# Optimization experiments

Hardware: AMD Instinct MI355X
Metric: run time of the kernel (lower is better)

Reference implementation:

```python
import jax, jax.numpy as jnp
import numpy as np


def setup_inputs() -> dict:
    key = jax.random.key(0)
    B, C, H, W = 16, 512, 56, 56
    heads, agent, win = 8, 49, 56
    ks = jax.random.split(key, 16)
    std = 0.02
    tn = lambda k, s: jax.random.truncated_normal(k, -2.0, 2.0, s, jnp.float32) * std
    return {
        "x": jax.random.normal(ks[0], (B, C, H, W), jnp.float32),
        "H": H,
        "W": W,
        "q_w": jax.random.normal(ks[1], (C, C), jnp.float32) * (C ** -0.5),
        "kv_w": jax.random.normal(ks[2], (2 * C, C), jnp.float32) * (C ** -0.5),
        "proj_w": jax.random.normal(ks[3], (C, C), jnp.float32) * (C ** -0.5),
        "proj_b": jnp.zeros((C,), jnp.float32),
        "dwc_w": jax.random.normal(ks[4], (C, 1, 3, 3), jnp.float32) * (1.0 / 3.0),
        "dwc_b": jnp.zeros((C,), jnp.float32),
        "an_bias": tn(ks[5], (heads, agent, 7, 7)),
        "na_bias": tn(ks[6], (heads, agent, 7, 7)),
        "ah_bias": tn(ks[7], (1, heads, agent, win, 1)),
        "aw_bias": tn(ks[8], (1, heads, agent, 1, win)),
        "ha_bias": tn(ks[9], (1, heads, win, 1, agent)),
        "wa_bias": tn(ks[10], (1, heads, 1, win, agent)),
    }


def reference(x, H, W, q_w, kv_w, proj_w, proj_b, dwc_w, dwc_b,
              an_bias, na_bias, ah_bias, aw_bias, ha_bias, wa_bias):
    B, C, H1, W1 = x.shape
    heads, agent = an_bias.shape[0], an_bias.shape[1]
    hd = C // heads
    scale = hd ** -0.5
    n = H1 * W1
    pool = int(agent ** 0.5)  # 7

    # NOTE: original torch code does x.view(B, H1*W1, C) on an NCHW tensor:
    # a raw row-major reshape, reproduced faithfully here.
    xf = x.reshape(B, n, C)

    q = xf @ q_w.T                       # [B, n, C]
    kv = xf @ kv_w.T                     # [B, n, 2C]
    k, v = kv[..., :C], kv[..., C:]

    # agent tokens: adaptive avg pool of q (as HxW image) to pool x pool (exact blocks)
    q_img = q.reshape(B, H, W, C)
    agent_tokens = q_img.reshape(B, pool, H // pool, pool, W // pool, C).mean(axis=(2, 4))
    agent_tokens = agent_tokens.reshape(B, agent, C)

    qh = q.reshape(B, n, heads, hd).transpose(0, 2, 1, 3)            # [B,h,n,d]
    kh = k.reshape(B, n, heads, hd).transpose(0, 2, 1, 3)            # [B,h,n,d]
    vh = v.reshape(B, n, heads, hd).transpose(0, 2, 1, 3)            # [B,h,n,d]
    ah = agent_tokens.reshape(B, agent, heads, hd).transpose(0, 2, 1, 3)  # [B,h,a,d]

    # stage 1: agent -> kv attention, with interpolated + separable position bias
    pb1 = jax.image.resize(an_bias, (heads, agent, H, W), 'bilinear').reshape(1, heads, agent, n)
    pb2 = (ah_bias + aw_bias).reshape(1, heads, agent, n)
    agent_logits = jnp.einsum('bhad,bhnd->bhan', ah * scale, kh) + pb1 + pb2
    agent_attn = jax.nn.softmax(agent_logits, axis=-1)
    agent_v = jnp.einsum('bhan,bhnd->bhad', agent_attn, vh)          # [B,h,a,d]

    # stage 2: query -> agent attention
    ab1 = jax.image.resize(na_bias, (heads, agent, H, W), 'bilinear').reshape(1, heads, agent, n)
    ab1 = ab1.transpose(0, 1, 3, 2)                                  # [1,h,n,a]
    ab2 = (ha_bias + wa_bias).reshape(1, heads, n, agent)
    q_logits = jnp.einsum('bhnd,bhad->bhna', qh * scale, ah) + ab1 + ab2
    q_attn = jax.nn.softmax(q_logits, axis=-1)
    out = jnp.einsum('bhna,bhad->bhnd', q_attn, agent_v)
    out = out.transpose(0, 2, 1, 3).reshape(B, n, C)

    # depthwise-conv residual on v (sr_ratio == 1: no interpolate)
    v_img = v.reshape(B, H, W, C).transpose(0, 3, 1, 2)              # [B,C,H,W]
    dwc = jax.lax.conv_general_dilated(
        v_img, dwc_w, window_strides=(1, 1), padding='SAME',
        feature_group_count=C, dimension_numbers=('NCHW', 'OIHW', 'NCHW'))
    dwc = dwc + dwc_b[None, :, None, None]
    out = out + dwc.transpose(0, 2, 3, 1).reshape(B, n, C)

    out = out @ proj_w.T + proj_b
    return out.reshape(B, C, H1, W1)
```

## Files before the change

kernel.cpp:

```cpp
#include <hip/hip_runtime.h>
#include <math.h>

#define B_ 16
#define C_ 512
#define Nn 3136
#define HEADS 8
#define HD 64
#define AG 49
#define Mrows (B_ * Nn)

typedef unsigned short ushortT;
typedef __attribute__((ext_vector_type(8))) short bf16x8;
typedef __attribute__((ext_vector_type(4))) float f32x4;

#define MFMA16(a, b, c) __builtin_amdgcn_mfma_f32_16x16x32_bf16((a), (b), (c), 0, 0, 0)

__device__ inline float bf2f(ushortT u) { return __uint_as_float(((unsigned)u) << 16); }
__device__ inline ushortT f2bf(float f) {
    unsigned x = __float_as_uint(f);
    unsigned r = (x + 0x7fffu + ((x >> 16) & 1u)) >> 16;
    return (ushortT)r;
}
__device__ inline f32x4 fzero4() { f32x4 z = {0.f, 0.f, 0.f, 0.f}; return z; }

__device__ inline void gl_lds16(const ushortT* g, ushortT* l) {
    __builtin_amdgcn_global_load_lds(
        (const __attribute__((address_space(1))) void*)g,
        (__attribute__((address_space(3))) void*)l, 16, 0, 0);
}

#define VMCNT(n) asm volatile("s_waitcnt vmcnt(" #n ")" ::: "memory")
#define LGKM0_SB() { asm volatile("s_waitcnt lgkmcnt(0)" ::: "memory"); \
                     __builtin_amdgcn_sched_barrier(0); }
#define BAR() __builtin_amdgcn_s_barrier()

__global__ void cvt_weights(const float* __restrict__ qw, const float* __restrict__ kvw,
                            const float* __restrict__ pw, const float* __restrict__ dwcw,
                            ushortT* __restrict__ Wqkv, ushortT* __restrict__ Wp,
                            float* __restrict__ wT) {
    int g = blockIdx.x * 256 + threadIdx.x;
    if (g < 196608) {
        const float* src = (g < 65536) ? &qw[(size_t)g * 4] : &kvw[(size_t)(g - 65536) * 4];
        float4 v = *(const float4*)src;
        *(ushort4*)&Wqkv[(size_t)g * 4] =
            make_ushort4(f2bf(v.x), f2bf(v.y), f2bf(v.z), f2bf(v.w));
    } else if (g < 262144) {
        float4 v = *(const float4*)&pw[(size_t)(g - 196608) * 4];
        *(ushort4*)&Wp[(size_t)(g - 196608) * 4] =
            make_ushort4(f2bf(v.x), f2bf(v.y), f2bf(v.z), f2bf(v.w));
    } else {
        int gg = g - 262144;
        if (gg < 4608) { int c = gg & 511, tap = gg >> 9; wT[gg] = dwcw[c * 9 + tap]; }
    }
}

template <int MB, int NL>
__device__ __forceinline__ void quad(f32x4 (&acc)[8][4], const bf16x8 (&af)[4][2],
                                     const bf16x8 (&bf)[4][2]) {
#pragma unroll
    for (int m = 0; m < 4; ++m)
#pragma unroll
        for (int n = 0; n < 2; ++n) {
            acc[MB + m][NL + n] = MFMA16(af[m][0], bf[NL + n][0], acc[MB + m][NL + n]);
            acc[MB + m][NL + n] = MFMA16(af[m][1], bf[NL + n][1], acc[MB + m][NL + n]);
        }
}

__global__ __launch_bounds__(512, 2)
void gemm_f32a(const float* __restrict__ A32, const ushortT* __restrict__ Bw,
               ushortT* __restrict__ out, int N, int nbn) {
    __shared__ __align__(16) ushortT As[2][16384];
    __shared__ __align__(16) ushortT Bs[2][16384];
    const int t = threadIdx.x, lane = t & 63, wid = t >> 6;
    const int chunk = (int)gridDim.x >> 3;
    const int id2 = ((int)blockIdx.x & 7) * chunk + ((int)blockIdx.x >> 3);
    const int by = id2 / nbn, bx = id2 - by * nbn;
    const int m0 = by * 256, n0 = bx * 256;
    const int wm = wid >> 2, wn = wid & 3;

    const int rl0 = t >> 3;
    const int kg = t & 7;
    const int wkg = kg ^ (rl0 & 7);
    const float* gAr = A32 + (size_t)(m0 + rl0) * 512 + kg * 8;
    const int dA0 = rl0 * 64 + wkg * 8;
    const int rb0 = (rl0 & 31) + ((rl0 >> 5) << 6);
    const int rb1 = rb0 + 128;
    const ushortT* gB0 = Bw + (size_t)(n0 + rb0) * 512 + wkg * 8;
    const ushortT* gB1 = Bw + (size_t)(n0 + rb1) * 512 + wkg * 8;
    const int gbu = ((wid * 8) & 31) + (((wid * 8) >> 5) << 6);
    const int bB0 = gbu * 64;
    const int bB1 = bB0 + 8192;

#define ISSB(bufi, ro, ko) { gl_lds16(gB0 + (ro) * 512 + (ko), &Bs[bufi][bB0 + (ro) * 64]); \
                             gl_lds16(gB1 + (ro) * 512 + (ko), &Bs[bufi][bB1 + (ro) * 64]); }
#define CVTW(bufi) { \
    _Pragma("unroll") \
    for (int j = 0; j < 4; ++j) { \
        bf16x8 w; \
        w[0]=(short)f2bf(pa[j][0].x); w[1]=(short)f2bf(pa[j][0].y); \
        w[2]=(short)f2bf(pa[j][0].z); w[3]=(short)f2bf(pa[j][0].w); \
        w[4]=(short)f2bf(pa[j][1].x); w[5]=(short)f2bf(pa[j][1].y); \
        w[6]=(short)f2bf(pa[j][1].z); w[7]=(short)f2bf(pa[j][1].w); \
        *(bf16x8*)&As[bufi][dA0 + j * 4096] = w; \
    } }

    f32x4 acc[8][4];
#pragma unroll
    for (int i = 0; i < 8; ++i)
#pragma unroll
        for (int j = 0; j < 4; ++j) acc[i][j] = fzero4();

    const int r15 = lane & 15, kq16 = lane >> 4;
    const int rA = wm * 128 + r15;
    const int rB = wn * 64 + r15;
    const int sw0 = ((kq16) ^ (r15 & 7)) << 3;
    const int sw1 = ((4 + kq16) ^ (r15 & 7)) << 3;

    float4 pa[4][2];
#pragma unroll
    for (int j = 0; j < 4; ++j) {
        const float* s = gAr + (size_t)j * 64 * 512;
        pa[j][0] = *(const float4*)s; pa[j][1] = *(const float4*)(s + 4);
    }
    ISSB(0, 0, 0); ISSB(0, 32, 0);
    CVTW(0);
    __syncthreads();

    bf16x8 af[4][2], bf[4][2];
    int cur = 0;
    for (int kt = 0; kt < 8; ++kt) {
        const ushortT* Ac = As[cur];
        const ushortT* Bc = Bs[cur];
        const int nb = cur ^ 1;
        const int ko = (kt + 1) * 64;
        const bool pre = (kt < 7);
        if (pre) {
#pragma unroll
            for (int j = 0; j < 4; ++j) {
                const float* s = gAr + (size_t)j * 64 * 512 + ko;
                pa[j][0] = *(const float4*)s; pa[j][1] = *(const float4*)(s + 4);
            }
            ISSB(nb, 0, ko); ISSB(nb, 32, ko);
        }
#pragma unroll
        for (int mt = 0; mt < 4; ++mt) {
            af[mt][0] = *(const bf16x8*)&Ac[(rA + mt * 16) * 64 + sw0];
            af[mt][1] = *(const bf16x8*)&Ac[(rA + mt * 16) * 64 + sw1];
        }
#pragma unroll
        for (int nt = 0; nt < 2; ++nt) {
            bf[nt][0] = *(const bf16x8*)&Bc[(rB + nt * 16) * 64 + sw0];
            bf[nt][1] = *(const bf16x8*)&Bc[(rB + nt * 16) * 64 + sw1];
        }
        __builtin_amdgcn_s_setprio(1);
        quad<0, 0>(acc, af, bf);
        __builtin_amdgcn_s_setprio(0);
#pragma unroll
        for (int nt = 2; nt < 4; ++nt) {
            bf[nt][0] = *(const bf16x8*)&Bc[(rB + nt * 16) * 64 + sw0];
            bf[nt][1] = *(const bf16x8*)&Bc[(rB + nt * 16) * 64 + sw1];
        }
        __builtin_amdgcn_s_setprio(1);
        quad<0, 2>(acc, af, bf);
        __builtin_amdgcn_s_setprio(0);
#pragma unroll
        for (int mt = 0; mt < 4; ++mt) {
            af[mt][0] = *(const bf16x8*)&Ac[(rA + 64 + mt * 16) * 64 + sw0];
            af[mt][1] = *(const bf16x8*)&Ac[(rA + 64 + mt * 16) * 64 + sw1];
        }
        __builtin_amdgcn_s_setprio(1);
        quad<4, 0>(acc, af, bf);
        quad<4, 2>(acc, af, bf);
        __builtin_amdgcn_s_setprio(0);
        if (pre) { CVTW(nb); }
        __syncthreads();
        cur ^= 1;
    }
#undef ISSB
#undef CVTW

    const int cn = r15, rg = kq16 << 2;
#pragma unroll
    for (int mt = 0; mt < 8; ++mt) {
        int mrow = m0 + wm * 128 + mt * 16 + rg;
#pragma unroll
        for (int nt = 0; nt < 4; ++nt) {
            int ncol = n0 + wn * 64 + nt * 16 + cn;
#pragma unroll
            for (int r = 0; r < 4; ++r)
                out[(size_t)(mrow + r) * N + ncol] = f2bf(acc[mt][nt][r]);
        }
    }
}

template <typename TO>
__global__ __launch_bounds__(512, 2)
void gemm256(const ushortT* __restrict__ A, const ushortT* __restrict__ Bw,
             const float* __restrict__ bias, TO* __restrict__ out,
             int N, int nbn) {
    __shared__ __align__(16) ushortT As[2][16384];
    __shared__ __align__(16) ushortT Bs[2][16384];
    const int t = threadIdx.x, lane = t & 63, wid = t >> 6;
    const int chunk = (int)gridDim.x >> 3;
    const int id2 = ((int)blockIdx.x & 7) * chunk + ((int)blockIdx.x >> 3);
    const int by = id2 / nbn, bx = id2 - by * nbn;
    const int m0 = by * 256, n0 = bx * 256;
    const int wm = wid >> 2, wn = wid & 3;

    const int rl0 = t >> 3;
    const int skg = (t & 7) ^ (rl0 & 7);
    const int ra0 = rl0 & 63;
    const int ra1 = (rl0 & 63) + 128;
    const int rb0 = (rl0 & 31) + ((rl0 >> 5) << 6);
    const int rb1 = rb0 + 128;
    const ushortT* gA0 = A + (size_t)(m0 + ra0) * 512 + skg * 8;
    const ushortT* gA1 = A + (size_t)(m0 + ra1) * 512 + skg * 8;
    const ushortT* gB0 = Bw + (size_t)(n0 + rb0) * 512 + skg * 8;
    const ushortT* gB1 = Bw + (size_t)(n0 + rb1) * 512 + skg * 8;
    const int bA0 = wid * 512;
    const int bA1 = wid * 512 + 8192;
    const int gbu = ((wid * 8) & 31) + (((wid * 8) >> 5) << 6);
    const int bB0 = gbu * 64;
    const int bB1 = bB0 + 8192;

#define ISSA(bufi, ro, ko) { gl_lds16(gA0 + (ro) * 512 + (ko), &As[bufi][bA0 + (ro) * 64]); \
                             gl_lds16(gA1 + (ro) * 512 + (ko), &As[bufi][bA1 + (ro) * 64]); }
#define ISSB(bufi, ro, ko) { gl_lds16(gB0 + (ro) * 512 + (ko), &Bs[bufi][bB0 + (ro) * 64]); \
                             gl_lds16(gB1 + (ro) * 512 + (ko), &Bs[bufi][bB1 + (ro) * 64]); }

    f32x4 acc[8][4];
#pragma unroll
    for (int i = 0; i < 8; ++i)
#pragma unroll
        for (int j = 0; j < 4; ++j) acc[i][j] = fzero4();

    const int r15 = lane & 15, kq16 = lane >> 4;
    const int rA = wm * 128 + r15;
    const int rB = wn * 64 + r15;
    const int sw0 = ((kq16) ^ (r15 & 7)) << 3;
    const int sw1 = ((4 + kq16) ^ (r15 & 7)) << 3;

    ISSA(0, 0, 0); ISSA(0, 64, 0);
    ISSB(0, 0, 0); ISSB(0, 32, 0);
    VMCNT(0);
    BAR();

    bf16x8 af[4][2], bf[4][2];
    for (int kt = 0; kt < 8; ++kt) {
        const ushortT* Ac = As[kt & 1];
        const ushortT* Bc = Bs[kt & 1];
        const int nb = (kt + 1) & 1;
        const int ko = (kt + 1) * 64;
        const bool pre = (kt < 7);
#pragma unroll
        for (int mt = 0; mt < 4; ++mt) {
            af[mt][0] = *(const bf16x8*)&Ac[(rA + mt * 16) * 64 + sw0];
            af[mt][1] = *(const bf16x8*)&Ac[(rA + mt * 16) * 64 + sw1];
        }
#pragma unroll
        for (int nt = 0; nt < 2; ++nt) {
            bf[nt][0] = *(const bf16x8*)&Bc[(rB + nt * 16) * 64 + sw0];
            bf[nt][1] = *(const bf16x8*)&Bc[(rB + nt * 16) * 64 + sw1];
        }
        if (pre) { ISSA(nb, 0, ko); ISSA(nb, 64, ko); }
        BAR(); LGKM0_SB();
        __builtin_amdgcn_s_setprio(1);
        quad<0, 0>(acc, af, bf);
        __builtin_amdgcn_s_setprio(0);
        BAR();
#pragma unroll
        for (int nt = 2; nt < 4; ++nt) {
            bf[nt][0] = *(const bf16x8*)&Bc[(rB + nt * 16) * 64 + sw0];
            bf[nt][1] = *(const bf16x8*)&Bc[(rB + nt * 16) * 64 + sw1];
        }
        if (pre) { ISSB(nb, 0, ko); ISSB(nb, 32, ko); }
        BAR(); LGKM0_SB();
        __builtin_amdgcn_s_setprio(1);
        quad<0, 2>(acc, af, bf);
        __builtin_amdgcn_s_setprio(0);
        BAR();
#pragma unroll
        for (int mt = 0; mt < 4; ++mt) {
            af[mt][0] = *(const bf16x8*)&Ac[(rA + 64 + mt * 16) * 64 + sw0];
            af[mt][1] = *(const bf16x8*)&Ac[(rA + 64 + mt * 16) * 64 + sw1];
        }
        BAR(); LGKM0_SB();
        __builtin_amdgcn_s_setprio(1);
        quad<4, 0>(acc, af, bf);
        __builtin_amdgcn_s_setprio(0);
        BAR();
        __builtin_amdgcn_s_setprio(1);
        quad<4, 2>(acc, af, bf);
        __builtin_amdgcn_s_setprio(0);
        if (pre) { VMCNT(0); }
        BAR();
    }
#undef ISSA
#undef ISSB

    const int cn = r15, rg = kq16 << 2;
#pragma unroll
    for (int mt = 0; mt < 8; ++mt) {
        int mrow = m0 + wm * 128 + mt * 16 + rg;
#pragma unroll
        for (int nt = 0; nt < 4; ++nt) {
            int ncol = n0 + wn * 64 + nt * 16 + cn;
            float bv = bias ? bias[ncol] : 0.f;
#pragma unroll
            for (int r = 0; r < 4; ++r) {
                float v = acc[mt][nt][r] + bv;
                if (sizeof(TO) == 2) ((ushortT*)out)[(size_t)(mrow + r) * N + ncol] = f2bf(v);
                else                 ((float*)out)[(size_t)(mrow + r) * N + ncol] = v;
            }
        }
    }
}

__global__ __launch_bounds__(256)
void agent_pool(const ushortT* __restrict__ qkv, float* __restrict__ at) {
    __shared__ float red[256][9];
    int t = threadIdx.x;
    int ba = blockIdx.x;
    int b = ba / AG, a = ba % AG;
    int c8 = (t & 63) << 3, qr = t >> 6;
    int p1 = a / 7, p2 = a % 7;
    float s[8] = {};
#pragma unroll
    for (int pp = 0; pp < 16; ++pp) {
        int pos = (qr << 4) + pp;
        int i = (p1 * 8 + (pos >> 3)) * 56 + p2 * 8 + (pos & 7);
        bf16x8 u = *(const bf16x8*)&qkv[(size_t)(b * Nn + i) * 1536 + c8];
#pragma unroll
        for (int j = 0; j < 8; ++j) s[j] += bf2f((ushortT)u[j]);
    }
#pragma unroll
    for (int j = 0; j < 8; ++j) red[t][j] = s[j];
    __syncthreads();
    if (t < 64) {
        float* o = &at[((size_t)(b * AG + a) << 9) + (t << 3)];
#pragma unroll
        for (int j = 0; j < 8; ++j)
            o[j] = (red[t][j] + red[t + 64][j] + red[t + 128][j] + red[t + 192][j])
                   * (1.f / 64.f);
    }
}

__device__ inline float bilin7(const float* __restrict__ p, int y, int x) {
    float fy = fminf(fmaxf(y * 0.125f - 0.4375f, 0.f), 6.f);
    float fx = fminf(fmaxf(x * 0.125f - 0.4375f, 0.f), 6.f);
    int y0 = (int)fy; float ty = fy - y0; int y1 = min(y0 + 1, 6);
    int x0 = (int)fx; float tx = fx - x0; int x1 = min(x0 + 1, 6);
    float v00 = p[y0 * 7 + x0], v01 = p[y0 * 7 + x1];
    float v10 = p[y1 * 7 + x0], v11 = p[y1 * 7 + x1];
    return (1.f - ty) * ((1.f - tx) * v00 + tx * v01) + ty * ((1.f - tx) * v10 + tx * v11);
}

__global__ void bias_k(const float* __restrict__ an, const float* __restrict__ ahb,
                       const float* __restrict__ awb, const float* __restrict__ na,
                       const float* __restrict__ hab, const float* __restrict__ wab,
                       ushortT* __restrict__ b1, ushortT* __restrict__ b2) {
    int g = blockIdx.x * 256 + threadIdx.x;
    const int NT = HEADS * AG * Nn;
    if (g < NT) {
        int i = g % Nn; int a = (g / Nn) % AG; int h = g / (AG * Nn);
        int y = i / 56, x = i % 56;
        b1[g] = f2bf(bilin7(an + (h * AG + a) * 49, y, x)
                     + ahb[(h * AG + a) * 56 + y] + awb[(h * AG + a) * 56 + x]);
    } else {
        g -= NT; if (g >= NT) return;
        int a = g % AG; int i = (g / AG) % Nn; int h = g / (AG * Nn);
        int y = i / 56, x = i % 56;
        b2[g] = f2bf(bilin7(na + (h * AG + a) * 49, y, x)
                     + hab[(h * 56 + y) * AG + a] + wab[(h * 56 + x) * AG + a]);
    }
}

__global__ void zero2(float* __restrict__ num, int n1, float* __restrict__ den, int n2) {
    int g = blockIdx.x * 256 + threadIdx.x;
    if (g < n1) num[g] = 0.f;
    else if (g - n1 < n2) den[g - n1] = 0.f;
}

__global__ __launch_bounds__(256)
void agent_av_fused(const ushortT* __restrict__ qkv, const float* __restrict__ at,
                    const ushortT* __restrict__ b1, float* __restrict__ num,
                    float* __restrict__ den) {
    __shared__ __align__(16) ushortT ah_s[64 * 72];
    __shared__ __align__(16) ushortT vt[64 * 72];
    __shared__ __align__(16) ushortT p_s[64 * 72];
    const int t = threadIdx.x, lane = t & 63, wid = t >> 6;
    const int bh = blockIdx.y, b = bh >> 3, h = bh & 7;
    for (int idx = t; idx < 512; idx += 256) {
        int a = idx >> 3, d8 = (idx & 7) << 3;
        bf16x8 tmp;
        if (a < AG) {
            const float* p = &at[((size_t)(b * AG + a) << 9) + (h << 6) + d8];
#pragma unroll
            for (int j = 0; j < 8; ++j) tmp[j] = (short)f2bf(p[j] * 0.125f);
        } else {
#pragma unroll
            for (int j = 0; j < 8; ++j) tmp[j] = 0;
        }
        *(bf16x8*)&ah_s[a * 72 + d8] = tmp;
    }
    __syncthreads();
    const int r15 = lane & 15, kq = (lane >> 4) << 3;
    const int rbase = (lane >> 4) << 2;
    bf16x8 af[4][2];
#pragma unroll
    for (int mt = 0; mt < 4; ++mt)
#pragma unroll
        for (int ks = 0; ks < 2; ++ks)
            af[mt][ks] = *(const bf16x8*)&ah_s[(mt * 16 + r15) * 72 + ks * 32 + kq];

    f32x4 accn[4];
#pragma unroll
    for (int nt = 0; nt < 4; ++nt) accn[nt] = fzero4();
    float denl[4][4];
#pragma unroll
    for (int mt = 0; mt < 4; ++mt)
#pragma unroll
        for (int r = 0; r < 4; ++r) denl[mt][r] = 0.f;

    const int i0b = blockIdx.x * 448;
    const int svi = t >> 2, svd = (t & 3) << 4;
    for (int cc = 0; cc < 7; ++cc) {
        const int i0 = i0b + cc * 64;
        {
            const ushortT* vp = &qkv[(size_t)(b * Nn + i0 + svi) * 1536 + 1024 + (h << 6) + svd];
            bf16x8 u0 = *(const bf16x8*)vp;
            bf16x8 u1 = *(const bf16x8*)(vp + 8);
#pragma unroll
            for (int j = 0; j < 8; ++j) {
                vt[(svd + j) * 72 + svi]     = (ushortT)u0[j];
                vt[(svd + 8 + j) * 72 + svi] = (ushortT)u1[j];
            }
        }
        {
            const int iw = i0 + wid * 16;
            const ushortT* kp = &qkv[(size_t)(b * Nn + iw + r15) * 1536 + 512 + (h << 6) + kq];
            bf16x8 bk0 = *(const bf16x8*)kp;
            bf16x8 bk1 = *(const bf16x8*)(kp + 32);
            f32x4 sacc[4];
#pragma unroll
            for (int mt = 0; mt < 4; ++mt) {
                sacc[mt] = MFMA16(af[mt][0], bk0, fzero4());
                sacc[mt] = MFMA16(af[mt][1], bk1, sacc[mt]);
            }
            const int ic = iw + r15;
#pragma unroll
            for (int mt = 0; mt < 4; ++mt)
#pragma unroll
                for (int r = 0; r < 4; ++r) {
                    int a = mt * 16 + rbase + r;
                    float e = 0.f;
                    if (a < AG)
                        e = __expf(sacc[mt][r] + bf2f(b1[(size_t)(h * AG + a) * Nn + ic]));
                    denl[mt][r] += e;
                    p_s[a * 72 + wid * 16 + r15] = f2bf(e);
                }
        }
        __syncthreads();
        {
            bf16x8 ap0 = *(const bf16x8*)&p_s[(wid * 16 + r15) * 72 + kq];
            bf16x8 ap1 = *(const bf16x8*)&p_s[(wid * 16 + r15) * 72 + 32 + kq];
#pragma unroll
            for (int nt = 0; nt < 4; ++nt) {
                bf16x8 bv0 = *(const bf16x8*)&vt[(nt * 16 + r15) * 72 + kq];
                bf16x8 bv1 = *(const bf16x8*)&vt[(nt * 16 + r15) * 72 + 32 + kq];
                accn[nt] = MFMA16(ap0, bv0, accn[nt]);
                accn[nt] = MFMA16(ap1, bv1, accn[nt]);
            }
        }
        __syncthreads();
    }
#pragma unroll
    for (int r = 0; r < 4; ++r) {
        int a = wid * 16 + rbase + r;
        if (a < AG) {
#pragma unroll
            for (int nt = 0; nt < 4; ++nt)
                atomicAdd(&num[((size_t)(bh * AG + a) << 6) + nt * 16 + r15],
                          accn[nt][r]);
        }
    }
#pragma unroll
    for (int mt = 0; mt < 4; ++mt)
#pragma unroll
        for (int r = 0; r < 4; ++r) {
            float s = denl[mt][r];
#pragma unroll
            for (int off = 8; off >= 1; off >>= 1) s += __shfl_xor(s, off);
            if (r15 == 0) {
                int a = mt * 16 + rbase + r;
                if (a < AG) atomicAdd(&den[bh * AG + a], s);
            }
        }
}

__global__ __launch_bounds__(256)
void q_attn_mfma(const ushortT* __restrict__ qkv, const float* __restrict__ at,
                 const float* __restrict__ num, const float* __restrict__ den,
                 const ushortT* __restrict__ b2, ushortT* __restrict__ attn) {
    __shared__ __align__(16) ushortT ah_s[64 * 72];
    __shared__ __align__(16) ushortT avT[64 * 72];
    __shared__ __align__(16) ushortT p_s[4][16 * 72];
    int t = threadIdx.x, lane = t & 63, wid = t >> 6;
    int bh = blockIdx.y, b = bh >> 3, h = bh & 7;
    for (int idx = t; idx < 512; idx += 256) {
        int a = idx >> 3, d8 = (idx & 7) << 3;
        bf16x8 tmp;
        if (a < AG) {
            const float* p = &at[((size_t)(b * AG + a) << 9) + (h << 6) + d8];
#pragma unroll
            for (int j = 0; j < 8; ++j) tmp[j] = (short)f2bf(p[j] * 0.125f);
        } else {
#pragma unroll
            for (int j = 0; j < 8; ++j) tmp[j] = 0;
        }
        *(bf16x8*)&ah_s[a * 72 + d8] = tmp;
    }
    for (int idx = t; idx < 4096; idx += 256) {
        int a = idx >> 6, d = idx & 63;
        float v = 0.f;
        if (a < AG)
            v = num[((size_t)(bh * AG + a) << 6) + d] / den[bh * AG + a];
        avT[d * 72 + a] = f2bf(v);
    }
    __syncthreads();
    int r15 = lane & 15, kq = (lane >> 4) << 3;
    bf16x8 bah[4][2], bav[4][2];
#pragma unroll
    for (int nt = 0; nt < 4; ++nt)
#pragma unroll
        for (int ks = 0; ks < 2; ++ks) {
            bah[nt][ks] = *(const bf16x8*)&ah_s[(nt * 16 + r15) * 72 + ks * 32 + kq];
            bav[nt][ks] = *(const bf16x8*)&avT[(nt * 16 + r15) * 72 + ks * 32 + kq];
        }
    ushortT* psw = p_s[wid];
    int i0b = blockIdx.x * 448;
    int rbase = (lane >> 4) << 2;
    for (int tt = 0; tt < 7; ++tt) {
        int i0 = i0b + (wid * 7 + tt) * 16;
        const ushortT* qp = &qkv[(size_t)(b * Nn + i0 + r15) * 1536 + (h << 6) + kq];
        bf16x8 aq0 = *(const bf16x8*)qp;
        bf16x8 aq1 = *(const bf16x8*)(qp + 32);
        f32x4 lg[4];
#pragma unroll
        for (int nt = 0; nt < 4; ++nt) {
            lg[nt] = MFMA16(aq0, bah[nt][0], fzero4());
            lg[nt] = MFMA16(aq1, bah[nt][1], lg[nt]);
        }
        float p4[4][4];
#pragma unroll
        for (int r = 0; r < 4; ++r) {
            int i = i0 + rbase + r;
            float vals[4]; float sm = 0.f;
#pragma unroll
            for (int nt = 0; nt < 4; ++nt) {
                int a = nt * 16 + r15;
                float e = 0.f;
                if (a < AG)
                    e = __expf(lg[nt][r] + bf2f(b2[(size_t)(h * Nn + i) * AG + a]));
                vals[nt] = e; sm += e;
            }
#pragma unroll
            for (int off = 8; off >= 1; off >>= 1) sm += __shfl_xor(sm, off);
            float inv = 1.f / sm;
#pragma unroll
            for (int nt = 0; nt < 4; ++nt) p4[nt][r] = vals[nt] * inv;
        }
#pragma unroll
        for (int nt = 0; nt < 4; ++nt)
#pragma unroll
            for (int r = 0; r < 4; ++r)
                psw[(rbase + r) * 72 + nt * 16 + r15] = f2bf(p4[nt][r]);
        bf16x8 ap0 = *(const bf16x8*)&psw[r15 * 72 + kq];
        bf16x8 ap1 = *(const bf16x8*)&psw[r15 * 72 + 32 + kq];
        f32x4 ov[4];
#pragma unroll
        for (int nt = 0; nt < 4; ++nt) {
            ov[nt] = MFMA16(ap0, bav[nt][0], fzero4());
            ov[nt] = MFMA16(ap1, bav[nt][1], ov[nt]);
        }
#pragma unroll
        for (int r = 0; r < 4; ++r) {
            int i = i0 + rbase + r;
            ushortT* op = &attn[(size_t)(b * Nn + i) * C_ + (h << 6)];
#pragma unroll
            for (int nt = 0; nt < 4; ++nt)
                op[nt * 16 + r15] = f2bf(ov[nt][r]);
        }
    }
}

__global__ void dwc_add_v(const ushortT* __restrict__ qkv, const float* __restrict__ wT,
                          const float* __restrict__ bb, ushortT* __restrict__ attn) {
    int g = blockIdx.x * 256 + threadIdx.x;
    int c8 = (g & 63) << 3;
    int bi = g >> 6;
    int i = bi % Nn;
    int y = i / 56, x = i % 56;
    float acc[8];
    {
        float4 b0 = *(const float4*)&bb[c8];
        float4 b1 = *(const float4*)&bb[c8 + 4];
        acc[0] = b0.x; acc[1] = b0.y; acc[2] = b0.z; acc[3] = b0.w;
        acc[4] = b1.x; acc[5] = b1.y; acc[6] = b1.z; acc[7] = b1.w;
    }
#pragma unroll
    for (int dy = -1; dy <= 1; ++dy) {
        int yy = y + dy; if (yy < 0 || yy > 55) continue;
#pragma unroll
        for (int dx = -1; dx <= 1; ++dx) {
            int xx = x + dx; if (xx < 0 || xx > 55) continue;
            const ushortT* vp = &qkv[(size_t)(bi + dy * 56 + dx) * 1536 + 1024 + c8];
            ushort4 u0 = *(const ushort4*)vp;
            ushort4 u1 = *(const ushort4*)(vp + 4);
            const float* wp = &wT[((dy + 1) * 3 + dx + 1) * 512 + c8];
            float4 w0 = *(const float4*)wp;
            float4 w1 = *(const float4*)(wp + 4);
            acc[0] += bf2f(u0.x) * w0.x; acc[1] += bf2f(u0.y) * w0.y;
            acc[2] += bf2f(u0.z) * w0.z; acc[3] += bf2f(u0.w) * w0.w;
            acc[4] += bf2f(u1.x) * w1.x; acc[5] += bf2f(u1.y) * w1.y;
            acc[6] += bf2f(u1.z) * w1.z; acc[7] += bf2f(u1.w) * w1.w;
        }
    }
    ushortT* op = &attn[(size_t)bi * C_ + c8];
    ushort4 a0 = *(const ushort4*)op;
    ushort4 a1 = *(const ushort4*)(op + 4);
    ushort4 o0 = make_ushort4(f2bf(bf2f(a0.x) + acc[0]), f2bf(bf2f(a0.y) + acc[1]),
                              f2bf(bf2f(a0.z) + acc[2]), f2bf(bf2f(a0.w) + acc[3]));
    ushort4 o1 = make_ushort4(f2bf(bf2f(a1.x) + acc[4]), f2bf(bf2f(a1.y) + acc[5]),
                              f2bf(bf2f(a1.z) + acc[6]), f2bf(bf2f(a1.w) + acc[7]));
    *(ushort4*)op = o0; *(ushort4*)(op + 4) = o1;
}

extern "C" void kernel_launch(void* const* d_in, const int* in_sizes, int n_in,
                              void* d_out, int out_size, void* d_ws, size_t ws_size,
                              hipStream_t stream) {
    const float* x      = (const float*)d_in[0];
    const float* q_w    = (const float*)d_in[3];
    const float* kv_w   = (const float*)d_in[4];
    const float* proj_w = (const float*)d_in[5];
    const float* proj_b = (const float*)d_in[6];
    const float* dwc_w  = (const float*)d_in[7];
    const float* dwc_b  = (const float*)d_in[8];
    const float* an_b   = (const float*)d_in[9];
    const float* na_b   = (const float*)d_in[10];
    const float* ah_b   = (const float*)d_in[11];
    const float* aw_b   = (const float*)d_in[12];
    const float* ha_b   = (const float*)d_in[13];
    const float* wa_b   = (const float*)d_in[14];
    float* out = (float*)d_out;

    char* ws = (char*)d_ws;
    ushortT* R    = (ushortT*)(ws);
    ushortT* qkv  = (ushortT*)(ws + 51380224);
    ushortT* Wqkv = (ushortT*)(ws + 205520896);
    ushortT* Wp   = (ushortT*)(ws + 207093760);
    float*   wT   = (float*)(ws + 207618048);
    float*   at   = (float*)(ws + 207636480);
    ushortT* b1   = (ushortT*)(ws + 209242112);
    ushortT* b2   = (ushortT*)(ws + 211700736);
    float*   num  = (float*)(ws + 214159360);
    float*   den  = (float*)(ws + 215764992);
    ushortT* attn = R;

    cvt_weights<<<1042, 256, 0, stream>>>(q_w, kv_w, proj_w, dwc_w, Wqkv, Wp, wT);
    gemm_f32a<<<1176, 512, 0, stream>>>(x, Wqkv, qkv, 1536, 6);
    agent_pool<<<784, 256, 0, stream>>>(qkv, at);
    bias_k<<<9604, 256, 0, stream>>>(an_b, ah_b, aw_b, na_b, ha_b, wa_b, b1, b2);
    zero2<<<1593, 256, 0, stream>>>(num, B_ * HEADS * AG * HD, den, B_ * HEADS * AG);
    agent_av_fused<<<dim3(7, 128), 256, 0, stream>>>(qkv, at, b1, num, den);
    q_attn_mfma<<<dim3(7, 128), 256, 0, stream>>>(qkv, at, num, den, b2, attn);
    dwc_add_v<<<12544, 256, 0, stream>>>(qkv, wT, dwc_b, attn);
    gemm256<float><<<392, 512, 0, stream>>>(attn, Wp, proj_b, out, 512, 2);
}
```

Before: 522.3 us.

## Replace atomic accumulation with per-split partial buffers and store agent tokens in bf16

The agent-to-token kernel now splits the 49 chunks of 64 tokens into 4 slices (13+12+12+12) instead of 7, and writes partial numerator and denominator sums to separate buffers rather than using global atomics. The zero-init kernel is removed, and the query-attention kernel sums the 4 partials itself. Agent tokens are stored pre-scaled in bf16 by the pooling kernel, which removes the per-block float-to-bf16 conversion and the scaling step. In exchange there are fewer blocks in the agent kernel (512 vs 896), so less parallelism, plus extra partial reads in q_attn.

```diff
diff --git a/kernel.cpp b/kernel.cpp
--- a/kernel.cpp
+++ b/kernel.cpp
@@ -317,7 +317,7 @@
 }
 
 __global__ __launch_bounds__(256)
-void agent_pool(const ushortT* __restrict__ qkv, float* __restrict__ at) {
+void agent_pool(const ushortT* __restrict__ qkv, ushortT* __restrict__ at) {
     __shared__ float red[256][9];
     int t = threadIdx.x;
     int ba = blockIdx.x;
@@ -337,11 +337,11 @@
     for (int j = 0; j < 8; ++j) red[t][j] = s[j];
     __syncthreads();
     if (t < 64) {
-        float* o = &at[((size_t)(b * AG + a) << 9) + (t << 3)];
+        ushortT* o = &at[((size_t)(b * AG + a) << 9) + (t << 3)];
 #pragma unroll
         for (int j = 0; j < 8; ++j)
-            o[j] = (red[t][j] + red[t + 64][j] + red[t + 128][j] + red[t + 192][j])
-                   * (1.f / 64.f);
+            o[j] = f2bf((red[t][j] + red[t + 64][j] + red[t + 128][j] + red[t + 192][j])
+                        * (1.f / 512.f));
     }
 }
 
@@ -375,28 +375,22 @@
     }
 }
 
-__global__ void zero2(float* __restrict__ num, int n1, float* __restrict__ den, int n2) {
-    int g = blockIdx.x * 256 + threadIdx.x;
-    if (g < n1) num[g] = 0.f;
-    else if (g - n1 < n2) den[g - n1] = 0.f;
-}
-
 __global__ __launch_bounds__(256)
-void agent_av_fused(const ushortT* __restrict__ qkv, const float* __restrict__ at,
-                    const ushortT* __restrict__ b1, float* __restrict__ num,
-                    float* __restrict__ den) {
+void agent_av_fused(const ushortT* __restrict__ qkv, const ushortT* __restrict__ at,
+                    const ushortT* __restrict__ b1, float* __restrict__ num_p,
+                    float* __restrict__ den_p) {
     __shared__ __align__(16) ushortT ah_s[64 * 72];
     __shared__ __align__(16) ushortT vt[64 * 72];
     __shared__ __align__(16) ushortT p_s[64 * 72];
     const int t = threadIdx.x, lane = t & 63, wid = t >> 6;
-    const int bh = blockIdx.y, b = bh >> 3, h = bh & 7;
+    const int bx = blockIdx.x, bh = blockIdx.y, b = bh >> 3, h = bh & 7;
+    const int cs = bx ? (13 + 12 * (bx - 1)) : 0;
+    const int ce = cs + (bx ? 12 : 13);
     for (int idx = t; idx < 512; idx += 256) {
         int a = idx >> 3, d8 = (idx & 7) << 3;
         bf16x8 tmp;
         if (a < AG) {
-            const float* p = &at[((size_t)(b * AG + a) << 9) + (h << 6) + d8];
-#pragma unroll
-            for (int j = 0; j < 8; ++j) tmp[j] = (short)f2bf(p[j] * 0.125f);
+            tmp = *(const bf16x8*)&at[((size_t)(b * AG + a) << 9) + (h << 6) + d8];
         } else {
 #pragma unroll
             for (int j = 0; j < 8; ++j) tmp[j] = 0;
@@ -422,10 +416,9 @@
 #pragma unroll
         for (int r = 0; r < 4; ++r) denl[mt][r] = 0.f;
 
-    const int i0b = blockIdx.x * 448;
     const int svi = t >> 2, svd = (t & 3) << 4;
-    for (int cc = 0; cc < 7; ++cc) {
-        const int i0 = i0b + cc * 64;
+    for (int cc = cs; cc < ce; ++cc) {
+        const int i0 = cc * 64;
         {
             const ushortT* vp = &qkv[(size_t)(b * Nn + i0 + svi) * 1536 + 1024 + (h << 6) + svd];
             bf16x8 u0 = *(const bf16x8*)vp;
@@ -480,10 +473,11 @@
         if (a < AG) {
 #pragma unroll
             for (int nt = 0; nt < 4; ++nt)
-                atomicAdd(&num[((size_t)(bh * AG + a) << 6) + nt * 16 + r15],
-                          accn[nt][r]);
-        }
-    }
+                num_p[(((size_t)bx * 128 + bh) * AG + a) * 64 + nt * 16 + r15] =
+                    accn[nt][r];
+        }
+    }
+    float* dsc = (float*)vt;
 #pragma unroll
     for (int mt = 0; mt < 4; ++mt)
 #pragma unroll
@@ -491,40 +485,52 @@
             float s = denl[mt][r];
 #pragma unroll
             for (int off = 8; off >= 1; off >>= 1) s += __shfl_xor(s, off);
-            if (r15 == 0) {
-                int a = mt * 16 + rbase + r;
-                if (a < AG) atomicAdd(&den[bh * AG + a], s);
-            }
-        }
+            if (r15 == 0) dsc[wid * 64 + mt * 16 + rbase + r] = s;
+        }
+    __syncthreads();
+    if (t < 64)
+        den_p[((size_t)bx * 128 + bh) * 64 + t] =
+            dsc[t] + dsc[64 + t] + dsc[128 + t] + dsc[192 + t];
 }
 
 __global__ __launch_bounds__(256)
-void q_attn_mfma(const ushortT* __restrict__ qkv, const float* __restrict__ at,
-                 const float* __restrict__ num, const float* __restrict__ den,
+void q_attn_mfma(const ushortT* __restrict__ qkv, const ushortT* __restrict__ at,
+                 const float* __restrict__ num_p, const float* __restrict__ den_p,
                  const ushortT* __restrict__ b2, ushortT* __restrict__ attn) {
     __shared__ __align__(16) ushortT ah_s[64 * 72];
     __shared__ __align__(16) ushortT avT[64 * 72];
     __shared__ __align__(16) ushortT p_s[4][16 * 72];
+    __shared__ float den_s[64];
     int t = threadIdx.x, lane = t & 63, wid = t >> 6;
     int bh = blockIdx.y, b = bh >> 3, h = bh & 7;
     for (int idx = t; idx < 512; idx += 256) {
         int a = idx >> 3, d8 = (idx & 7) << 3;
         bf16x8 tmp;
         if (a < AG) {
-            const float* p = &at[((size_t)(b * AG + a) << 9) + (h << 6) + d8];
-#pragma unroll
-            for (int j = 0; j < 8; ++j) tmp[j] = (short)f2bf(p[j] * 0.125f);
+            tmp = *(const bf16x8*)&at[((size_t)(b * AG + a) << 9) + (h << 6) + d8];
         } else {
 #pragma unroll
             for (int j = 0; j < 8; ++j) tmp[j] = 0;
         }
         *(bf16x8*)&ah_s[a * 72 + d8] = tmp;
     }
+    if (t < 64) {
+        den_s[t] = den_p[((size_t)0 * 128 + bh) * 64 + t]
+                 + den_p[((size_t)1 * 128 + bh) * 64 + t]
+                 + den_p[((size_t)2 * 128 + bh) * 64 + t]
+                 + den_p[((size_t)3 * 128 + bh) * 64 + t];
+    }
+    __syncthreads();
     for (int idx = t; idx < 4096; idx += 256) {
         int a = idx >> 6, d = idx & 63;
         float v = 0.f;
-        if (a < AG)
-            v = num[((size_t)(bh * AG + a) << 6) + d] / den[bh * AG + a];
+        if (a < AG) {
+            float s = num_p[(((size_t)0 * 128 + bh) * AG + a) * 64 + d]
+                    + num_p[(((size_t)1 * 128 + bh) * AG + a) * 64 + d]
+                    + num_p[(((size_t)2 * 128 + bh) * AG + a) * 64 + d]
+                    + num_p[(((size_t)3 * 128 + bh) * AG + a) * 64 + d];
+            v = s / den_s[a];
+        }
         avT[d * 72 + a] = f2bf(v);
     }
     __syncthreads();
@@ -655,25 +661,23 @@
     float* out = (float*)d_out;
 
     char* ws = (char*)d_ws;
-    ushortT* R    = (ushortT*)(ws);
-    ushortT* qkv  = (ushortT*)(ws + 51380224);
-    ushortT* Wqkv = (ushortT*)(ws + 205520896);
-    ushortT* Wp   = (ushortT*)(ws + 207093760);
-    float*   wT   = (float*)(ws + 207618048);
-    float*   at   = (float*)(ws + 207636480);
-    ushortT* b1   = (ushortT*)(ws + 209242112);
-    ushortT* b2   = (ushortT*)(ws + 211700736);
-    float*   num  = (float*)(ws + 214159360);
-    float*   den  = (float*)(ws + 215764992);
-    ushortT* attn = R;
+    ushortT* attn  = (ushortT*)(ws);
+    ushortT* qkv   = (ushortT*)(ws + 51380224);
+    ushortT* Wqkv  = (ushortT*)(ws + 205520896);
+    ushortT* Wp    = (ushortT*)(ws + 207093760);
+    float*   wT    = (float*)(ws + 207618048);
+    ushortT* at    = (ushortT*)(ws + 207636480);
+    ushortT* b1    = (ushortT*)(ws + 208439296);
+    ushortT* b2    = (ushortT*)(ws + 210897920);
+    float*   num_p = (float*)(ws + 213356544);
+    float*   den_p = (float*)(ws + 219779072);
 
     cvt_weights<<<1042, 256, 0, stream>>>(q_w, kv_w, proj_w, dwc_w, Wqkv, Wp, wT);
     gemm_f32a<<<1176, 512, 0, stream>>>(x, Wqkv, qkv, 1536, 6);
     agent_pool<<<784, 256, 0, stream>>>(qkv, at);
     bias_k<<<9604, 256, 0, stream>>>(an_b, ah_b, aw_b, na_b, ha_b, wa_b, b1, b2);
-    zero2<<<1593, 256, 0, stream>>>(num, B_ * HEADS * AG * HD, den, B_ * HEADS * AG);
-    agent_av_fused<<<dim3(7, 128), 256, 0, stream>>>(qkv, at, b1, num, den);
-    q_attn_mfma<<<dim3(7, 128), 256, 0, stream>>>(qkv, at, num, den, b2, attn);
+    agent_av_fused<<<dim3(4, 128), 256, 0, stream>>>(qkv, at, b1, num_p, den_p);
+    q_attn_mfma<<<dim3(7, 128), 256, 0, stream>>>(qkv, at, num_p, den_p, b2, attn);
     dwc_add_v<<<12544, 256, 0, stream>>>(qkv, wT, dwc_b, attn);
     gemm256<float><<<392, 512, 0, stream>>>(attn, Wp, proj_b, out, 512, 2);
 }
```

Measured after the change: 518.8 us. About the same (-0.7%).
